# Kernel optimization log

Measured on AMD Instinct MI355X. Metric: run time of the kernel, lower is better.

The kernel has to match this reference:

```python
import jax, jax.numpy as jnp
import numpy as np

START_IDX = 1  # PAD_IDX = 0, END_IDX = 2 (unused in teacher-forcing path)
B, N, F = 16, 49, 1024
H, E, V = 1024, 1024, 15000
S, W = 5, 12


def setup_inputs() -> dict:
    key = jax.random.key(0)
    ks = jax.random.split(key, 16)
    def w(k, shape, s=0.02):
        return jax.random.normal(k, shape, dtype=jnp.float32) * s
    emb = w(ks[0], (V, E)).at[0].set(0.0)  # padding_idx = 0
    return dict(
        features=jax.random.normal(ks[1], (B, N, F), dtype=jnp.float32),
        reports=jax.random.randint(ks[2], (B, S, W), 0, V),
        attn_w1=w(ks[3], (F + H, H)), attn_b1=jnp.zeros((H,), jnp.float32),
        attn_w2=w(ks[4], (H, 1)), attn_b2=jnp.zeros((1,), jnp.float32),
        s_wih=w(ks[5], (4 * H, F)), s_whh=w(ks[6], (4 * H, H)),
        s_bih=jnp.zeros((4 * H,), jnp.float32), s_bhh=jnp.zeros((4 * H,), jnp.float32),
        stop_w=w(ks[7], (H, 1)), stop_b=jnp.zeros((1,), jnp.float32),
        emb=emb,
        w_wih=w(ks[8], (4 * H, E)), w_whh=w(ks[9], (4 * H, H)),
        w_bih=jnp.zeros((4 * H,), jnp.float32), w_bhh=jnp.zeros((4 * H,), jnp.float32),
        fc_w=w(ks[10], (H, V)), fc_b=jnp.zeros((V,), jnp.float32),
    )


def _lstm_cell(x, h, c, wih, whh, bih, bhh):
    # PyTorch LSTMCell: gates ordered i, f, g, o
    gates = x @ wih.T + h @ whh.T + (bih + bhh)
    i, f, g, o = jnp.split(gates, 4, axis=-1)
    c = jax.nn.sigmoid(f) * c + jax.nn.sigmoid(i) * jnp.tanh(g)
    h = jax.nn.sigmoid(o) * jnp.tanh(c)
    return h, c


def _attention(features, h, w1, b1, w2, b2):
    # features [B,N,F], h [B,H] -> additive 2-layer attention over N locations
    b, n, _ = features.shape
    hcat = jnp.broadcast_to(h[:, None, :], (b, n, h.shape[-1]))
    x = jnp.concatenate([features, hcat], axis=-1)           # [B,N,F+H]
    e = (jnp.tanh(x @ w1 + b1) @ w2 + b2)[..., 0]            # [B,N]
    scores = jax.nn.softmax(e, axis=-1)
    att = jnp.einsum('bn,bnf->bf', scores, features)          # [B,F]
    return att, scores


def _forward(features, reports, attn_w1, attn_b1, attn_w2, attn_b2,
             s_wih, s_whh, s_bih, s_bhh, stop_w, stop_b, emb,
             w_wih, w_whh, w_bih, w_bhh, fc_w, fc_b):
    bsz = features.shape[0]
    h0 = jnp.zeros((bsz, s_whh.shape[-1]), features.dtype)
    att0, _ = _attention(features, h0, attn_w1, attn_b1, attn_w2, attn_b2)
    start_emb = jnp.broadcast_to(emb[START_IDX][None, :], (bsz, emb.shape[-1]))

    def sentence_step(carry, reports_i):   # reports_i: [W, B] teacher-forcing tokens
        h, c, att = carry
        h, c = _lstm_cell(att, h, c, s_wih, s_whh, s_bih, s_bhh)
        czero = jnp.zeros_like(h)

        def word_step(wc, idx):
            hw, cw, inp = wc
            hw, cw = _lstm_cell(inp, hw, cw, w_wih, w_whh, w_bih, w_bhh)
            pred = hw @ fc_w + fc_b                           # [B,V]
            return (hw, cw, emb[idx]), pred

        # word LSTM initialized with h=topic, c=0; first input = <start> embedding
        _, preds = jax.lax.scan(word_step, (h, czero, start_emb), reports_i)  # [W,B,V]
        stop = jax.nn.sigmoid(h @ stop_w + stop_b)[:, 0]      # [B]
        att, scores = _attention(features, h, attn_w1, attn_b1, attn_w2, attn_b2)
        return (h, c, att), (preds, stop, scores)

    reports_sw = jnp.transpose(reports, (1, 2, 0))            # [S,W,B]
    _, (seq, stops, scores) = jax.lax.scan(sentence_step, (h0, h0, att0), reports_sw)
    seq_out = jnp.transpose(seq, (2, 0, 1, 3))                # [B,S,W,V]
    stops_out = jnp.transpose(stops, (1, 0))                  # [B,S]
    scores_out = jnp.transpose(scores, (1, 0, 2))             # [B,S,N]
    return seq_out, stops_out, scores_out


def reference(features, reports, attn_w1, attn_b1, attn_w2, attn_b2,
              s_wih, s_whh, s_bih, s_bhh, stop_w, stop_b, emb,
              w_wih, w_whh, w_bih, w_bhh, fc_w, fc_b):
    return _forward(features, reports, attn_w1, attn_b1, attn_w2, attn_b2,
                    s_wih, s_whh, s_bih, s_bhh, stop_w, stop_b, emb,
                    w_wih, w_whh, w_bih, w_bhh, fc_w, fc_b)
```

## Files before the change

### kernel.cpp

```cpp
#include <hip/hip_runtime.h>
#include <hip/hip_bf16.h>

#define B_  16
#define S_  5
#define W_  12
#define NL_ 49
#define H_  1024
#define V_  15000
#define SEQ_N   14400000
#define STOP_N  80
#define OUT_STOP (SEQ_N)
#define OUT_SCORE (SEQ_N + STOP_N)

typedef __attribute__((ext_vector_type(8))) short     short8;
typedef __attribute__((ext_vector_type(4))) float     f32x4;
typedef __attribute__((ext_vector_type(4))) unsigned int u32x4;
typedef __attribute__((ext_vector_type(4))) unsigned short us4;

#define OFF_FCWT   0ull
#define OFF_WWHHP  30720000ull
#define OFF_WWIHP  39108608ull
#define OFF_WSCATP 47497216ull
#define OFF_W1AT   64274432ull
#define OFF_W1BT   66371584ull
#define OFF_FBF    68468736ull
#define OFF_XIN    70074368ull
#define OFF_PF     72040448ull
#define OFF_XW     75251712ull
#define OFF_HBALL  90980352ull
#define OFF_HWBF0  92946432ull
#define OFF_HWBF1  93110272ull
#define OFF_ACAT1  93274112ull
#define OFF_H      93339648ull
#define OFF_EVAL   93405184ull
#define OFF_ACAT0  93408384ull
#define OFF_C      93473920ull
#define OFF_CW     93539456ull
#define OFF_HPROJ  93867136ull
#define WS_TOTAL   93932672ull
#define ZERO_BASE  OFF_ACAT0
#define ZERO_BYTES (524288ull)

__device__ __forceinline__ unsigned short f2bf(float x){
  unsigned u = __float_as_uint(x);
  u += 0x7fffu + ((u >> 16) & 1u);
  return (unsigned short)(u >> 16);
}
__device__ __forceinline__ float sigm(float x){ return 1.f/(1.f+expf(-x)); }

typedef __attribute__((address_space(3))) unsigned int  as3_u32;
typedef __attribute__((address_space(1))) const unsigned int as1_u32;

__device__ __forceinline__ void gl16(const void* g, void* l){
  __builtin_amdgcn_global_load_lds((as1_u32*)g, (as3_u32*)l, 16, 0, 0);
}

template<int ROWS,int CH,int NW>
__device__ __forceinline__ void stage_swz(const unsigned short* __restrict__ gbase, int grs,
                                          unsigned short* lds, int wid, int lane,
                                          int r0, int rmax){
  constexpr int RPI = 64/CH;
  constexpr int NISS = ROWS/RPI;
  const int r_in = lane / CH;
  const int cbp  = lane % CH;
  #pragma unroll
  for (int it = wid; it < NISS; it += NW){
    int rl = it*RPI + r_in;
    int gr = r0 + rl; gr = gr < rmax ? gr : rmax-1;
    int cb = cbp ^ (rl & 7);
    gl16(gbase + (size_t)gr*grs + cb*8, lds + it*RPI*CH*8);
  }
}

__device__ __forceinline__ void cvt_gate_blk(const float* __restrict__ src,
                                             unsigned short* __restrict__ dst,
                                             int blk, int dld, int doff){
  int idx = (blk*256 + threadIdx.x)*4;
  int n = idx >> 10, cc = idx & 1023;
  int gate = (n >> 4) & 3, j = ((n >> 6) << 4) | (n & 15);
  f32x4 v = *(const f32x4*)(src + ((size_t)(gate*1024 + j) << 10) + cc);
  us4 o; o[0]=f2bf(v[0]); o[1]=f2bf(v[1]); o[2]=f2bf(v[2]); o[3]=f2bf(v[3]);
  *(us4*)(dst + (size_t)n*dld + doff + cc) = o;
}

__global__ void k_prep(const float* __restrict__ features,
                       const float* __restrict__ w_whh, const float* __restrict__ w_wih,
                       const float* __restrict__ s_wih, const float* __restrict__ s_whh,
                       const float* __restrict__ emb, const int* __restrict__ reports,
                       unsigned short* __restrict__ FBF, unsigned short* __restrict__ WWHHP,
                       unsigned short* __restrict__ WWIHP, unsigned short* __restrict__ WSCATP,
                       unsigned short* __restrict__ XIN)
{
  int bx = blockIdx.x;
  if (bx < 784){
    int idx = (bx*256 + threadIdx.x)*4;
    f32x4 v = *(const f32x4*)(features + idx);
    us4 o; o[0]=f2bf(v[0]); o[1]=f2bf(v[1]); o[2]=f2bf(v[2]); o[3]=f2bf(v[3]);
    *(us4*)(FBF + idx) = o;
  } else if (bx < 784 + 4096){
    cvt_gate_blk(w_whh, WWHHP, bx - 784, 1024, 0);
  } else if (bx < 784 + 8192){
    cvt_gate_blk(w_wih, WWIHP, bx - (784 + 4096), 1024, 0);
  } else if (bx < 784 + 12288){
    cvt_gate_blk(s_wih, WSCATP, bx - (784 + 8192), 2048, 0);
  } else if (bx < 784 + 16384){
    cvt_gate_blk(s_whh, WSCATP, bx - (784 + 12288), 2048, 1024);
  } else {
    int m = bx - (784 + 16384);
    int w = m / 80, r = m % 80, s = r >> 4, b = r & 15;
    int tok = (w == 0) ? 1 : reports[b*60 + s*12 + (w-1)];
    const float* src = emb + ((size_t)tok << 10);
    int k = threadIdx.x * 4;
    f32x4 v = *(const f32x4*)(src + k);
    us4 o; o[0]=f2bf(v[0]); o[1]=f2bf(v[1]); o[2]=f2bf(v[2]); o[3]=f2bf(v[3]);
    *(us4*)(XIN + (size_t)m*1024 + k) = o;
  }
}

__global__ void k_transp_w1(const float* __restrict__ src,
                            unsigned short* __restrict__ W1AT, unsigned short* __restrict__ W1BT){
  __shared__ float t[32][33];
  unsigned short* dst = blockIdx.z ? W1BT : W1AT;
  int r0 = blockIdx.z * 1024;
  int rb = blockIdx.x*32, cb = blockIdx.y*32;
  int tx = threadIdx.x & 31, ty = threadIdx.x >> 5;
  for (int i = ty; i < 32; i += 8)
    t[i][tx] = src[(size_t)(r0 + rb + i)*1024 + cb + tx];
  __syncthreads();
  for (int i = ty; i < 32; i += 8)
    dst[(size_t)(cb + i)*1024 + rb + tx] = f2bf(t[tx][i]);
}

__global__ void k_transp(const float* __restrict__ src, int sld, int r0, int R, int Cc,
                         unsigned short* __restrict__ dst, int dld){
  __shared__ float t[32][33];
  int rb = blockIdx.x*32, cb = blockIdx.y*32;
  int tx = threadIdx.x & 31, ty = threadIdx.x >> 5;
  for (int i = ty; i < 32; i += 8){
    int r = rb + i, c = cb + tx;
    t[i][tx] = (r < R && c < Cc) ? src[(size_t)(r0 + r)*sld + c] : 0.f;
  }
  __syncthreads();
  for (int i = ty; i < 32; i += 8){
    int c = cb + i, r = rb + tx;
    if (c < Cc && r < R) dst[(size_t)c*dld + r] = f2bf(t[tx][i]);
  }
}

template<int BM,int BN,int BK,int WM,int WN,int EPI>
__global__ void k_gemm(const unsigned short* __restrict__ A, int lda,
                       const unsigned short* __restrict__ Bt, int ldb,
                       float* __restrict__ C, int ldc,
                       const float* __restrict__ bias,
                       int M, int N, int K)
{
  constexpr int NWV = WM*WN;
  constexpr int CH = BK/8;
  __shared__ __align__(16) unsigned short As[BM*BK];
  __shared__ __align__(16) unsigned short Bs[BN*BK];
  const int n0 = blockIdx.x * BN, m0 = blockIdx.y * BM;
  const int tid  = threadIdx.x;
  const int lane = tid & 63;
  const int wave = tid >> 6;
  constexpr int WROWS = BM/WM, WCOLS = BN/WN;
  constexpr int FM = WROWS/16, FN = WCOLS/16;
  const int wm = wave / WN, wn = wave % WN;
  const int g = lane >> 4, fr = lane & 15;
  const int sx = fr & 7;

  f32x4 acc[FM][FN];
  #pragma unroll
  for (int a=0;a<FM;a++)
    #pragma unroll
    for (int b=0;b<FN;b++) acc[a][b] = (f32x4){0.f,0.f,0.f,0.f};

  for (int k0 = 0; k0 < K; k0 += BK) {
    if (k0) __syncthreads();
    stage_swz<BM,CH,NWV>(A + k0, lda, As, wave, lane, m0, M);
    stage_swz<BN,CH,NWV>(Bt + k0, ldb, Bs, wave, lane, n0, N);
    __syncthreads();
    #pragma unroll
    for (int kk = 0; kk < BK; kk += 32) {
      const int so = ((kk/8 + g) ^ sx) * 8;
      short8 af[FM], bt[FN];
      #pragma unroll
      for (int fm=0; fm<FM; fm++)
        af[fm] = *(const short8*)(As + (wm*WROWS + fm*16 + fr)*BK + so);
      #pragma unroll
      for (int fn=0; fn<FN; fn++)
        bt[fn] = *(const short8*)(Bs + (wn*WCOLS + fn*16 + fr)*BK + so);
      #pragma unroll
      for (int fm=0; fm<FM; fm++)
        #pragma unroll
        for (int fn=0; fn<FN; fn++)
          acc[fm][fn] = __builtin_amdgcn_mfma_f32_16x16x32_bf16(af[fm], bt[fn], acc[fm][fn], 0, 0, 0);
    }
  }

  #pragma unroll
  for (int fm=0; fm<FM; fm++)
    #pragma unroll
    for (int fn=0; fn<FN; fn++)
      #pragma unroll
      for (int j=0; j<4; j++){
        int m = m0 + wm*WROWS + fm*16 + g*4 + j;
        int n = n0 + wn*WCOLS + fn*16 + fr;
        if (m < M && n < N) {
          float v = acc[fm][fn][j];
          if (EPI == 1 || EPI == 2) v += bias[n];
          if (EPI == 2) {
            int b = m & 15, s = (m >> 4) % 5, w = m / 80;
            __builtin_nontemporal_store(v, &C[(size_t)((b*5 + s)*12 + w)*V_ + n]);
          } else if (EPI == 3) {
            __builtin_nontemporal_store(v, &C[(size_t)m*ldc + n]);
          } else {
            C[(size_t)m*ldc + n] = v;
          }
        }
      }
}

template<int KH,int NI,int MB,int EPI>
__global__ void __launch_bounds__(64*KH) k_cell(
    const unsigned short* __restrict__ A, int lda,
    const unsigned short* __restrict__ Bt, int ldb,
    const float* __restrict__ Xg, int ldx,
    const float* __restrict__ bih, const float* __restrict__ bhh,
    float* __restrict__ cst,
    unsigned short* __restrict__ h1, int ldh1,
    unsigned short* __restrict__ h2,
    float* __restrict__ hf,
    float* __restrict__ C, int ldc)
{
  __shared__ __align__(16) unsigned short Bsw[KH*64*128];
  const int tid = threadIdx.x, lane = tid & 63, kh = tid >> 6;
  const int n0 = blockIdx.x * 64;
  const int g = lane >> 4, fr = lane & 15;
  unsigned short* myB = Bsw + kh*(64*128);
  const int cbp = lane & 15;

  f32x4 acc[MB][4];
  #pragma unroll
  for (int mb=0;mb<MB;mb++)
    #pragma unroll
    for (int fn=0;fn<4;fn++) acc[mb][fn] = (f32x4){0.f,0.f,0.f,0.f};

  #pragma unroll
  for (int i=0;i<NI;i++){
    const int kb = (kh*NI + i)*128;
    if (i) asm volatile("s_waitcnt lgkmcnt(0)" ::: "memory");
    #pragma unroll
    for (int it=0; it<16; ++it){
      int rl = it*4 + g;
      int cb = cbp ^ (rl & 7);
      gl16(Bt + (size_t)(n0+rl)*ldb + kb + cb*8, myB + it*512 + lane*8);
    }
    short8 afr[MB][4];
    #pragma unroll
    for (int mb=0;mb<MB;mb++)
      #pragma unroll
      for (int q=0;q<4;q++)
        afr[mb][q] = *(const short8*)(A + (size_t)(mb*16+fr)*lda + kb + q*32 + g*8);
    asm volatile("s_waitcnt vmcnt(0)" ::: "memory");
    #pragma unroll
    for (int q=0;q<4;q++){
      const int so = ((q*4 + g) ^ (fr & 7)) * 8;
      #pragma unroll
      for (int fn=0;fn<4;fn++){
        short8 bt = *(const short8*)(myB + (fn*16+fr)*128 + so);
        #pragma unroll
        for (int mb=0;mb<MB;mb++)
          acc[mb][fn] = __builtin_amdgcn_mfma_f32_16x16x32_bf16(afr[mb][q], bt, acc[mb][fn], 0, 0, 0);
      }
    }
  }

  constexpr int SR = MB*16 + 1;
  __syncthreads();
  float* rbuf = (float*)Bsw;
  if (kh > 0){
    float* dst = rbuf + ((kh-1)*64 + lane)*SR;
    #pragma unroll
    for (int mb=0;mb<MB;mb++)
      #pragma unroll
      for (int fn=0;fn<4;fn++)
        #pragma unroll
        for (int jj=0;jj<4;jj++)
          dst[mb*16 + fn*4 + jj] = acc[mb][fn][jj];
  }
  __syncthreads();
  if (kh == 0){
    #pragma unroll
    for (int q=1;q<KH;q++){
      const float* src = rbuf + ((q-1)*64 + lane)*SR;
      #pragma unroll
      for (int mb=0;mb<MB;mb++)
        #pragma unroll
        for (int fn=0;fn<4;fn++)
          #pragma unroll
          for (int jj=0;jj<4;jj++)
            acc[mb][fn][jj] += src[mb*16 + fn*4 + jj];
    }
    if (EPI == 2){
      #pragma unroll
      for (int mb=0;mb<MB;mb++)
        #pragma unroll
        for (int fn=0;fn<4;fn++)
          #pragma unroll
          for (int jj=0;jj<4;jj++)
            C[(size_t)(mb*16 + g*4 + jj)*ldc + n0 + fn*16 + fr] = acc[mb][fn][jj];
    } else {
      const int j  = (n0 >> 2) + fr;
      const int nb = n0 + fr;
      const float b0 = bih[j]        + bhh[j];
      const float b1 = bih[1024 + j] + bhh[1024 + j];
      const float b2 = bih[2048 + j] + bhh[2048 + j];
      const float b3 = bih[3072 + j] + bhh[3072 + j];
      #pragma unroll
      for (int mb=0;mb<MB;mb++)
        #pragma unroll
        for (int jj=0;jj<4;jj++){
          int m = mb*16 + g*4 + jj;
          float gi = acc[mb][0][jj] + b0;
          float gf = acc[mb][1][jj] + b1;
          float gg = acc[mb][2][jj] + b2;
          float go = acc[mb][3][jj] + b3;
          if (EPI == 0){
            const float* xg = Xg + (size_t)m*ldx + nb;
            gi += xg[0]; gf += xg[16]; gg += xg[32]; go += xg[48];
          }
          float cn = sigm(gf)*cst[m*1024 + j] + sigm(gi)*tanhf(gg);
          float hn = sigm(go)*tanhf(cn);
          cst[m*1024 + j] = cn;
          unsigned short hb = f2bf(hn);
          h1[(size_t)m*ldh1 + j] = hb;
          h2[(size_t)m*1024 + j] = hb;
          if (EPI == 1) hf[m*1024 + j] = hn;
        }
    }
  }
}

template<int INIT>
__global__ void __launch_bounds__(1024) k_attn2(
    const float* __restrict__ HPROJ, const float* __restrict__ PF,
    const float* __restrict__ w2, const float* __restrict__ features,
    const float* __restrict__ hF, const float* __restrict__ stop_w,
    const float* __restrict__ stop_b,
    unsigned short* __restrict__ att_out, float* __restrict__ outp, int s)
{
  __shared__ float hp[1024];
  __shared__ float ev[64];
  __shared__ float scs[NL_];
  __shared__ float red[16];
  const int b = blockIdx.x, tid = threadIdx.x;
  const int grp = tid >> 6, lane = tid & 63;

  hp[tid] = INIT ? 0.f : HPROJ[b*1024 + tid];
  __syncthreads();

  for (int n = grp; n < NL_; n += 16){
    const float* pf = PF + ((size_t)(b*NL_ + n) << 10);
    float p = 0.f;
    for (int k = lane*4; k < 1024; k += 256){
      f32x4 a = *(const f32x4*)(pf + k);
      f32x4 w = *(const f32x4*)(w2 + k);
      p += tanhf(a[0]+hp[k  ])*w[0] + tanhf(a[1]+hp[k+1])*w[1]
         + tanhf(a[2]+hp[k+2])*w[2] + tanhf(a[3]+hp[k+3])*w[3];
    }
    #pragma unroll
    for (int o = 32; o; o >>= 1) p += __shfl_down(p, o, 64);
    if (lane == 0) ev[n] = p;
  }
  __syncthreads();

  if (tid < 64){
    float e = (tid < NL_) ? ev[tid] : -1e30f;
    float mx = e;
    #pragma unroll
    for (int o = 32; o; o >>= 1) mx = fmaxf(mx, __shfl_xor(mx, o, 64));
    float ex = (tid < NL_) ? expf(e - mx) : 0.f;
    float dn = ex;
    #pragma unroll
    for (int o = 32; o; o >>= 1) dn += __shfl_xor(dn, o, 64);
    float sc = ex / dn;
    if (tid < NL_){
      scs[tid] = sc;
      if (!INIT) outp[OUT_SCORE + (b*5 + s)*NL_ + tid] = sc;
    }
  }
  __syncthreads();

  {
    float a = 0.f;
    const float* fb = features + (((size_t)(b*NL_)) << 10) + tid;
    #pragma unroll 7
    for (int n = 0; n < NL_; n++) a += scs[n] * fb[(size_t)n << 10];
    att_out[b*2048 + tid] = f2bf(a);
  }
  if (!INIT){
    float p = hF[b*1024 + tid] * stop_w[tid];
    #pragma unroll
    for (int o = 32; o; o >>= 1) p += __shfl_down(p, o, 64);
    if (lane == 0) red[grp] = p;
    __syncthreads();
    if (tid == 0){
      float t = 0.f;
      #pragma unroll
      for (int i = 0; i < 16; i++) t += red[i];
      outp[OUT_STOP + b*5 + s] = sigm(t + stop_b[0]);
    }
  }
}

extern "C" void kernel_launch(void* const* d_in, const int* in_sizes, int n_in,
                              void* d_out, int out_size, void* d_ws, size_t ws_size,
                              hipStream_t stream)
{
  const float* features = (const float*)d_in[0];
  const int*   reports  = (const int*)d_in[1];
  const float* attn_w1  = (const float*)d_in[2];
  const float* attn_b1  = (const float*)d_in[3];
  const float* attn_w2  = (const float*)d_in[4];
  const float* s_wih    = (const float*)d_in[6];
  const float* s_whh    = (const float*)d_in[7];
  const float* s_bih    = (const float*)d_in[8];
  const float* s_bhh    = (const float*)d_in[9];
  const float* stop_w   = (const float*)d_in[10];
  const float* stop_b   = (const float*)d_in[11];
  const float* emb      = (const float*)d_in[12];
  const float* w_wih    = (const float*)d_in[13];
  const float* w_whh    = (const float*)d_in[14];
  const float* w_bih    = (const float*)d_in[15];
  const float* w_bhh    = (const float*)d_in[16];
  const float* fc_w     = (const float*)d_in[17];
  const float* fc_b     = (const float*)d_in[18];
  float* out = (float*)d_out;
  char*  ws  = (char*)d_ws;
  if (ws_size < WS_TOTAL) return;

  unsigned short* FCWT   = (unsigned short*)(ws + OFF_FCWT);
  unsigned short* WWHHP  = (unsigned short*)(ws + OFF_WWHHP);
  unsigned short* WWIHP  = (unsigned short*)(ws + OFF_WWIHP);
  unsigned short* WSCATP = (unsigned short*)(ws + OFF_WSCATP);
  unsigned short* W1AT   = (unsigned short*)(ws + OFF_W1AT);
  unsigned short* W1BT   = (unsigned short*)(ws + OFF_W1BT);
  unsigned short* FBF    = (unsigned short*)(ws + OFF_FBF);
  unsigned short* XIN    = (unsigned short*)(ws + OFF_XIN);
  float*          PF     = (float*)(ws + OFF_PF);
  float*          XW     = (float*)(ws + OFF_XW);
  unsigned short* HBALL  = (unsigned short*)(ws + OFF_HBALL);
  unsigned short* HW0    = (unsigned short*)(ws + OFF_HWBF0);
  unsigned short* HW1    = (unsigned short*)(ws + OFF_HWBF1);
  unsigned short* ACAT0  = (unsigned short*)(ws + OFF_ACAT0);
  unsigned short* ACAT1  = (unsigned short*)(ws + OFF_ACAT1);
  float*          Hst    = (float*)(ws + OFF_H);
  float*          Cst    = (float*)(ws + OFF_C);
  float*          CW     = (float*)(ws + OFF_CW);
  float*          HPROJ  = (float*)(ws + OFF_HPROJ);

  hipMemsetAsync(ws + ZERO_BASE, 0, ZERO_BYTES, stream);

  k_prep<<<784 + 16384 + 960, 256, 0, stream>>>(features, w_whh, w_wih, s_wih, s_whh,
                                                emb, reports, FBF, WWHHP, WWIHP, WSCATP, XIN);
  k_transp_w1<<<dim3(32,32,2), 256, 0, stream>>>(attn_w1, W1AT, W1BT);
  k_transp<<<dim3(32,469), 256, 0, stream>>>(fc_w, 15000, 0, 1024, 15000, FCWT, 1024);

  k_gemm<64,64,128,2,2,1><<<dim3(16,13), 256, 0, stream>>>(FBF,1024, W1AT,1024, PF,1024, attn_b1, 784,1024,1024);
  k_gemm<64,128,128,2,2,3><<<dim3(32,15), 256, 0, stream>>>(XIN,1024, WWIHP,1024, XW,4096, nullptr, 960,4096,1024);

  k_attn2<1><<<16, 1024, 0, stream>>>(HPROJ, PF, attn_w2, features, Hst, stop_w, stop_b, ACAT0, out, 0);

  unsigned short* ACS[2] = {ACAT0, ACAT1};
  for (int s = 0; s < S_; s++){
    unsigned short* cur = ACS[s & 1];
    unsigned short* nxt = ACS[(s + 1) & 1];
    k_cell<4,4,1,1><<<64, 256, 0, stream>>>(
        cur, 2048, WSCATP, 2048, nullptr, 0, s_bih, s_bhh, Cst,
        nxt + 1024, 2048, HW0 + s*16*1024, Hst, nullptr, 0);
    k_cell<4,2,1,2><<<16, 256, 0, stream>>>(
        nxt + 1024, 2048, W1BT, 1024, nullptr, 0, nullptr, nullptr, nullptr,
        nullptr, 0, nullptr, nullptr, HPROJ, 1024);
    k_attn2<0><<<16, 1024, 0, stream>>>(HPROJ, PF, attn_w2, features, Hst, stop_w, stop_b, nxt, out, s);
  }

  unsigned short* HW[2] = {HW0, HW1};
  for (int w = 0; w < W_; w++){
    k_cell<4,2,5,0><<<64, 256, 0, stream>>>(
        HW[w & 1], 1024, WWHHP, 1024, XW + (size_t)w*80*4096, 4096, w_bih, w_bhh, CW,
        HW[(w + 1) & 1], 1024, HBALL + (size_t)w*80*1024, nullptr, nullptr, 0);
  }

  k_gemm<64,128,64,2,2,2><<<dim3(118,15), 256, 0, stream>>>(HBALL,1024, FCWT,1024, out,V_, fc_b, 960,15000,1024);
}
```

Before: 620.1 us.

## Double-buffer GEMM LDS staging and add XCD-aware tile swizzle for FC GEMM

Converts the bf16 MFMA GEMM to double-buffered LDS. The next K-tile's global-to-LDS loads are issued before computing the current tile, with explicit vmcnt waits and barriers. The big vocabulary projection GEMM is relaunched as a 1D grid whose block IDs are remapped so each XCD handles contiguous column panels for better L2 reuse. It also reduces BK to 64 for the prep GEMMs and changes the sentence cell launch to 8 waves per block. The cost is doubled LDS footprint, which may reduce occupancy, plus hand-tuned wait counts that depend on the load count per wave.

Result: no change. 625.6 us (+0.9%).

```diff
diff --git a/kernel.cpp b/kernel.cpp
--- a/kernel.cpp
+++ b/kernel.cpp
@@ -53,6 +53,15 @@
 
 __device__ __forceinline__ void gl16(const void* g, void* l){
   __builtin_amdgcn_global_load_lds((as1_u32*)g, (as3_u32*)l, 16, 0, 0);
+}
+
+template<int N> __device__ __forceinline__ void waitv(){
+  if constexpr (N==0)       asm volatile("s_waitcnt vmcnt(0)" ::: "memory");
+  else if constexpr (N==4)  asm volatile("s_waitcnt vmcnt(4)" ::: "memory");
+  else if constexpr (N==6)  asm volatile("s_waitcnt vmcnt(6)" ::: "memory");
+  else if constexpr (N==8)  asm volatile("s_waitcnt vmcnt(8)" ::: "memory");
+  else if constexpr (N==12) asm volatile("s_waitcnt vmcnt(12)" ::: "memory");
+  else                      asm volatile("s_waitcnt vmcnt(0)" ::: "memory");
 }
 
 template<int ROWS,int CH,int NW>
@@ -147,7 +156,7 @@
   }
 }
 
-template<int BM,int BN,int BK,int WM,int WN,int EPI>
+template<int BM,int BN,int BK,int WM,int WN,int EPI,int SWZ>
 __global__ void k_gemm(const unsigned short* __restrict__ A, int lda,
                        const unsigned short* __restrict__ Bt, int ldb,
                        float* __restrict__ C, int ldc,
@@ -156,9 +165,21 @@
 {
   constexpr int NWV = WM*WN;
   constexpr int CH = BK/8;
-  __shared__ __align__(16) unsigned short As[BM*BK];
-  __shared__ __align__(16) unsigned short Bs[BN*BK];
-  const int n0 = blockIdx.x * BN, m0 = blockIdx.y * BM;
+  static_assert((BM*CH/64) % NWV == 0 && (BN*CH/64) % NWV == 0, "stage divisibility");
+  constexpr int LPW = (BM*CH/64)/NWV + (BN*CH/64)/NWV;
+  __shared__ __align__(16) unsigned short As[2][BM*BK];
+  __shared__ __align__(16) unsigned short Bs[2][BN*BK];
+  int n0, m0;
+  if constexpr (SWZ){
+    int bid = blockIdx.x, xcd = bid & 7, lid = bid >> 3;
+    int P  = xcd < 6 ? 15 : 14;
+    int nb = xcd < 6 ? xcd*15 : 90 + (xcd-6)*14;
+    if (lid >= P*15) return;
+    n0 = (nb + lid/15) * BN;
+    m0 = (lid%15) * BM;
+  } else {
+    n0 = blockIdx.x * BN; m0 = blockIdx.y * BM;
+  }
   const int tid  = threadIdx.x;
   const int lane = tid & 63;
   const int wave = tid >> 6;
@@ -174,27 +195,39 @@
     #pragma unroll
     for (int b=0;b<FN;b++) acc[a][b] = (f32x4){0.f,0.f,0.f,0.f};
 
-  for (int k0 = 0; k0 < K; k0 += BK) {
-    if (k0) __syncthreads();
-    stage_swz<BM,CH,NWV>(A + k0, lda, As, wave, lane, m0, M);
-    stage_swz<BN,CH,NWV>(Bt + k0, ldb, Bs, wave, lane, n0, N);
-    __syncthreads();
+  stage_swz<BM,CH,NWV>(A, lda, As[0], wave, lane, m0, M);
+  stage_swz<BN,CH,NWV>(Bt, ldb, Bs[0], wave, lane, n0, N);
+
+  int t = 0;
+  for (int k0 = 0; k0 < K; k0 += BK, t ^= 1) {
+    if (k0 + BK < K) {
+      stage_swz<BM,CH,NWV>(A + k0 + BK, lda, As[t^1], wave, lane, m0, M);
+      stage_swz<BN,CH,NWV>(Bt + k0 + BK, ldb, Bs[t^1], wave, lane, n0, N);
+      waitv<LPW>();
+    } else {
+      waitv<0>();
+    }
+    __builtin_amdgcn_sched_barrier(0);
+    __builtin_amdgcn_s_barrier();
+    __builtin_amdgcn_sched_barrier(0);
     #pragma unroll
     for (int kk = 0; kk < BK; kk += 32) {
       const int so = ((kk/8 + g) ^ sx) * 8;
       short8 af[FM], bt[FN];
       #pragma unroll
       for (int fm=0; fm<FM; fm++)
-        af[fm] = *(const short8*)(As + (wm*WROWS + fm*16 + fr)*BK + so);
+        af[fm] = *(const short8*)(As[t] + (wm*WROWS + fm*16 + fr)*BK + so);
       #pragma unroll
       for (int fn=0; fn<FN; fn++)
-        bt[fn] = *(const short8*)(Bs + (wn*WCOLS + fn*16 + fr)*BK + so);
+        bt[fn] = *(const short8*)(Bs[t] + (wn*WCOLS + fn*16 + fr)*BK + so);
       #pragma unroll
       for (int fm=0; fm<FM; fm++)
         #pragma unroll
         for (int fn=0; fn<FN; fn++)
           acc[fm][fn] = __builtin_amdgcn_mfma_f32_16x16x32_bf16(af[fm], bt[fn], acc[fm][fn], 0, 0, 0);
     }
+    __builtin_amdgcn_sched_barrier(0);
+    __builtin_amdgcn_s_barrier();
   }
 
   #pragma unroll
@@ -466,8 +499,8 @@
   k_transp_w1<<<dim3(32,32,2), 256, 0, stream>>>(attn_w1, W1AT, W1BT);
   k_transp<<<dim3(32,469), 256, 0, stream>>>(fc_w, 15000, 0, 1024, 15000, FCWT, 1024);
 
-  k_gemm<64,64,128,2,2,1><<<dim3(16,13), 256, 0, stream>>>(FBF,1024, W1AT,1024, PF,1024, attn_b1, 784,1024,1024);
-  k_gemm<64,128,128,2,2,3><<<dim3(32,15), 256, 0, stream>>>(XIN,1024, WWIHP,1024, XW,4096, nullptr, 960,4096,1024);
+  k_gemm<64,64,64,2,2,1,0><<<dim3(16,13), 256, 0, stream>>>(FBF,1024, W1AT,1024, PF,1024, attn_b1, 784,1024,1024);
+  k_gemm<64,128,64,2,2,3,0><<<dim3(32,15), 256, 0, stream>>>(XIN,1024, WWIHP,1024, XW,4096, nullptr, 960,4096,1024);
 
   k_attn2<1><<<16, 1024, 0, stream>>>(HPROJ, PF, attn_w2, features, Hst, stop_w, stop_b, ACAT0, out, 0);
 
@@ -475,7 +508,7 @@
   for (int s = 0; s < S_; s++){
     unsigned short* cur = ACS[s & 1];
     unsigned short* nxt = ACS[(s + 1) & 1];
-    k_cell<4,4,1,1><<<64, 256, 0, stream>>>(
+    k_cell<8,2,1,1><<<64, 512, 0, stream>>>(
         cur, 2048, WSCATP, 2048, nullptr, 0, s_bih, s_bhh, Cst,
         nxt + 1024, 2048, HW0 + s*16*1024, Hst, nullptr, 0);
     k_cell<4,2,1,2><<<16, 256, 0, stream>>>(
@@ -491,5 +524,5 @@
         HW[(w + 1) & 1], 1024, HBALL + (size_t)w*80*1024, nullptr, nullptr, 0);
   }
 
-  k_gemm<64,128,64,2,2,2><<<dim3(118,15), 256, 0, stream>>>(HBALL,1024, FCWT,1024, out,V_, fc_b, 960,15000,1024);
-}
+  k_gemm<64,128,64,2,2,2,1><<<1800, 256, 0, stream>>>(HBALL,1024, FCWT,1024, out,V_, fc_b, 960,15000,1024);
+}
```
